# Performance work log

Measured on AMD Instinct MI355X. Metric: run time of the kernel, lower is better.

The kernel has to match this reference:

```python
import jax, jax.numpy as jnp
import numpy as np

B = 256
IN_F = 4096
OUT_F = 4096
NNZ_T = 500_000
NNZ_N = 100_000


def setup_inputs() -> dict:
    key = jax.random.key(0)
    k1, k2, k3, k4, k5, k6 = jax.random.split(key, 6)
    x = jax.random.normal(k1, (B, IN_F), dtype=jnp.float32)
    st_idx = jax.random.randint(k2, (2, NNZ_T), 0, OUT_F, dtype=jnp.int64)  # row in [0,OUT_F), col in [0,IN_F); both 4096
    st_vals = jax.random.normal(k3, (NNZ_T,), dtype=jnp.float32) * (1.0 / np.sqrt(IN_F))
    sn_idx = jax.random.randint(k4, (2, NNZ_N), 0, OUT_F, dtype=jnp.int64)
    sn_vals = jax.random.normal(k5, (NNZ_N,), dtype=jnp.float32) * (1.0 / np.sqrt(IN_F))
    b = jax.random.normal(k6, (OUT_F,), dtype=jnp.float32) * 0.01
    return {"x": x, "st_idx": st_idx, "st_vals": st_vals,
            "sn_idx": sn_idx, "sn_vals": sn_vals, "b": b}


def _spmm_t(x, idx, vals, out_features):
    """Compute x @ A^T where A is COO sparse with idx=(rows, cols), vals.
    A has shape (out_features, in_features). Returns (batch, out_features).
    Duplicate indices are summed, matching torch coalesce semantics."""
    rows, cols = idx[0], idx[1]
    contrib = x[:, cols] * vals[None, :]            # (B, nnz)
    y = jax.ops.segment_sum(contrib.T, rows, num_segments=out_features)  # (out, B)
    return y.T                                       # (B, out)


def reference(x, st_idx, st_vals, sn_idx, sn_vals, b):
    out_features = b.shape[0]
    # y = x @ (S_T + S_N)^T + b == x @ S_T^T + x @ S_N^T + b
    y = _spmm_t(x, st_idx, st_vals, out_features)
    y = y + _spmm_t(x, sn_idx, sn_vals, out_features)
    return y + b[None, :]
```

## Files before the change

### kernel.cpp

```cpp
#include <hip/hip_runtime.h>

#define IN_FT   4096
#define OUT_FT  4096
#define B_SZ    256
#define NNZ_T   500000
#define NNZ_N   100000
#define NNZ_TOT 600000
#define QTR_N   150000
#define QTR4    (QTR_N / 2)
#define ROWS_PB 64
#define QROW_CAP 256
#define ACC_LD  257

#define OFF_ENT  0u
#define OFF_XT   4800000u
#define OFF_FLAG 8994304u

__global__ __launch_bounds__(256) void k_init(const float* __restrict__ bias,
                                              float* __restrict__ out,
                                              const int* __restrict__ st_idx,
                                              const int* __restrict__ sn_idx,
                                              int* __restrict__ flag) {
    int i = blockIdx.x * 256 + threadIdx.x;
    float4* out4 = (float4*)out;
    const float4* bias4 = (const float4*)bias;
    out4[i] = bias4[i & 1023];
    if (blockIdx.x == 0) {
        __shared__ int nz_t, nz_n;
        if (threadIdx.x == 0) { nz_t = 0; nz_n = 0; }
        __syncthreads();
        if (st_idx[2 * threadIdx.x + 1] != 0) atomicAdd(&nz_t, 1);
        if (sn_idx[2 * threadIdx.x + 1] != 0) atomicAdd(&nz_n, 1);
        __syncthreads();
        if (threadIdx.x == 0) { flag[0] = (nz_t == 0); flag[1] = (nz_n == 0); }
    }
}

__global__ __launch_bounds__(256) void k_transpose(const float* __restrict__ in,
                                                   float* __restrict__ out,
                                                   int rows, int cols) {
    __shared__ float tile[32][33];
    int x0 = blockIdx.x * 32;
    int y0 = blockIdx.y * 32;
    int tx = threadIdx.x, ty = threadIdx.y;
    #pragma unroll
    for (int j = 0; j < 32; j += 8)
        tile[ty + j][tx] = in[(size_t)(y0 + ty + j) * cols + (x0 + tx)];
    __syncthreads();
    #pragma unroll
    for (int j = 0; j < 32; j += 8)
        out[(size_t)(x0 + ty + j) * rows + (y0 + tx)] = tile[tx][ty + j];
}

__device__ __forceinline__ void get_entry(int i,
                                          const int* __restrict__ st_idx,
                                          const float* __restrict__ st_vals,
                                          const int* __restrict__ sn_idx,
                                          const float* __restrict__ sn_vals,
                                          int stride_t, int stride_n,
                                          int& row, int& col, float& val) {
    if (i < NNZ_T) {
        row = st_idx[(size_t)i * stride_t];
        col = st_idx[(size_t)(NNZ_T + i) * stride_t];
        val = st_vals[i];
    } else {
        int j = i - NNZ_T;
        row = sn_idx[(size_t)j * stride_n];
        col = sn_idx[(size_t)(NNZ_N + j) * stride_n];
        val = sn_vals[j];
    }
}

__global__ __launch_bounds__(256) void k_pack(const int* __restrict__ st_idx,
                                              const float* __restrict__ st_vals,
                                              const int* __restrict__ sn_idx,
                                              const float* __restrict__ sn_vals,
                                              const int* __restrict__ flag,
                                              uint2* __restrict__ ent) {
    int i = blockIdx.x * 256 + threadIdx.x;
    if (i >= NNZ_TOT) return;
    int s_t = flag[0] ? 2 : 1, s_n = flag[1] ? 2 : 1;
    int row, col; float val;
    get_entry(i, st_idx, st_vals, sn_idx, sn_vals, s_t, s_n, row, col, val);
    ent[i] = make_uint2(((unsigned)row << 12) | (unsigned)col, __float_as_uint(val));
}

__global__ __launch_bounds__(1024) void k_gf(const float* __restrict__ xT,
                                             const uint2* __restrict__ ent,
                                             float* __restrict__ out) {
    extern __shared__ char smem[];
    uint2* queues = (uint2*)smem;
    float* acc    = (float*)smem;
    __shared__ int cnt_s[ROWS_PB];
    const int t = threadIdx.x;
    const int lane = t & 63;
    const int wave = t >> 6;
    const int qi = blockIdx.x & 3;
    const unsigned R0 = (unsigned)(blockIdx.x >> 2) * ROWS_PB;

    if (t < ROWS_PB) cnt_s[t] = 0;
    __syncthreads();

    const uint4* ep = (const uint4*)(ent + (size_t)qi * QTR_N);
    for (int i = t; i < QTR4; i += 1024) {
        uint4 e = ep[i];
        unsigned r0 = (e.x >> 12) - R0;
        if (r0 < (unsigned)ROWS_PB) {
            int p = atomicAdd(&cnt_s[r0], 1);
            if (p < QROW_CAP) queues[r0 * QROW_CAP + p] = make_uint2(e.x, e.y);
        }
        unsigned r1 = (e.z >> 12) - R0;
        if (r1 < (unsigned)ROWS_PB) {
            int p = atomicAdd(&cnt_s[r1], 1);
            if (p < QROW_CAP) queues[r1 * QROW_CAP + p] = make_uint2(e.z, e.w);
        }
    }
    __syncthreads();

    float4 av0 = {0.f,0.f,0.f,0.f}, av1 = av0, av2 = av0, av3 = av0;
    {
        const int q = wave * 4;
        const int n0 = min(cnt_s[q + 0], QROW_CAP);
        const int n1 = min(cnt_s[q + 1], QROW_CAP);
        const int n2 = min(cnt_s[q + 2], QROW_CAP);
        const int n3 = min(cnt_s[q + 3], QROW_CAP);
        const uint2* q0 = queues + (q + 0) * QROW_CAP;
        const uint2* q1 = queues + (q + 1) * QROW_CAP;
        const uint2* q2 = queues + (q + 2) * QROW_CAP;
        const uint2* q3 = queues + (q + 3) * QROW_CAP;
        const int nmax = max(max(n0, n1), max(n2, n3));
        #pragma unroll 2
        for (int j = 0; j < nmax; ++j) {
            uint2 e0 = (j < n0) ? q0[j] : make_uint2(0u, 0u);
            uint2 e1 = (j < n1) ? q1[j] : make_uint2(0u, 0u);
            uint2 e2 = (j < n2) ? q2[j] : make_uint2(0u, 0u);
            uint2 e3 = (j < n3) ? q3[j] : make_uint2(0u, 0u);
            const float4* p0 = (const float4*)(xT + (size_t)(e0.x & 4095u) * B_SZ);
            const float4* p1 = (const float4*)(xT + (size_t)(e1.x & 4095u) * B_SZ);
            const float4* p2 = (const float4*)(xT + (size_t)(e2.x & 4095u) * B_SZ);
            const float4* p3 = (const float4*)(xT + (size_t)(e3.x & 4095u) * B_SZ);
            float4 x0 = p0[lane];
            float4 x1 = p1[lane];
            float4 x2 = p2[lane];
            float4 x3 = p3[lane];
            float v0 = __uint_as_float(e0.y);
            float v1 = __uint_as_float(e1.y);
            float v2 = __uint_as_float(e2.y);
            float v3 = __uint_as_float(e3.y);
            av0.x = fmaf(v0, x0.x, av0.x); av0.y = fmaf(v0, x0.y, av0.y);
            av0.z = fmaf(v0, x0.z, av0.z); av0.w = fmaf(v0, x0.w, av0.w);
            av1.x = fmaf(v1, x1.x, av1.x); av1.y = fmaf(v1, x1.y, av1.y);
            av1.z = fmaf(v1, x1.z, av1.z); av1.w = fmaf(v1, x1.w, av1.w);
            av2.x = fmaf(v2, x2.x, av2.x); av2.y = fmaf(v2, x2.y, av2.y);
            av2.z = fmaf(v2, x2.z, av2.z); av2.w = fmaf(v2, x2.w, av2.w);
            av3.x = fmaf(v3, x3.x, av3.x); av3.y = fmaf(v3, x3.y, av3.y);
            av3.z = fmaf(v3, x3.z, av3.z); av3.w = fmaf(v3, x3.w, av3.w);
        }
    }
    __syncthreads();

    {
        float* a0 = acc + (wave * 4 + 0) * ACC_LD + 4 * lane;
        float* a1 = acc + (wave * 4 + 1) * ACC_LD + 4 * lane;
        float* a2 = acc + (wave * 4 + 2) * ACC_LD + 4 * lane;
        float* a3 = acc + (wave * 4 + 3) * ACC_LD + 4 * lane;
        a0[0] = av0.x; a0[1] = av0.y; a0[2] = av0.z; a0[3] = av0.w;
        a1[0] = av1.x; a1[1] = av1.y; a1[2] = av1.z; a1[3] = av1.w;
        a2[0] = av2.x; a2[1] = av2.y; a2[2] = av2.z; a2[3] = av2.w;
        a3[0] = av3.x; a3[1] = av3.y; a3[2] = av3.z; a3[3] = av3.w;
    }
    __syncthreads();

    #pragma unroll
    for (int k = 0; k < 16; ++k) {
        int cell = t + k * 1024;
        int rr = cell & 63, b = cell >> 6;
        unsafeAtomicAdd(&out[(size_t)b * OUT_FT + R0 + rr], acc[rr * ACC_LD + b]);
    }
}

extern "C" void kernel_launch(void* const* d_in, const int* in_sizes, int n_in,
                              void* d_out, int out_size, void* d_ws, size_t ws_size,
                              hipStream_t stream) {
    const float* x       = (const float*)d_in[0];
    const int*   st_idx  = (const int*)d_in[1];
    const float* st_vals = (const float*)d_in[2];
    const int*   sn_idx  = (const int*)d_in[3];
    const float* sn_vals = (const float*)d_in[4];
    const float* bias    = (const float*)d_in[5];
    float* out = (float*)d_out;

    char* ws = (char*)d_ws;
    uint2* ent  = (uint2*)(ws + OFF_ENT);
    float* xT   = (float*)(ws + OFF_XT);
    int*   flag = (int*)  (ws + OFF_FLAG);

    (void)hipFuncSetAttribute((const void*)k_gf,
                              hipFuncAttributeMaxDynamicSharedMemorySize, 131072);

    k_init<<<(B_SZ * OUT_FT / 4) / 256, 256, 0, stream>>>(bias, out, st_idx, sn_idx, flag);
    k_transpose<<<dim3(IN_FT / 32, B_SZ / 32), dim3(32, 8), 0, stream>>>(x, xT, B_SZ, IN_FT);
    k_pack<<<(NNZ_TOT + 255) / 256, 256, 0, stream>>>(st_idx, st_vals, sn_idx, sn_vals,
                                                      flag, ent);
    k_gf<<<256, 1024, 131072, stream>>>(xT, ent, out);
}
```

Before: 141.3 us.

## Batch gather loads in k_gf, zero-pad queues, halve LDS, stagger output atomics

The gather loop now runs in steps of four, fetching sixteen queue entries and then issuing sixteen independent xT float4 loads before any FMA, so more memory requests are in flight per wave. Queues are zero-filled up front, which lets padded slots read as column 0 with value 0 and removes the per-element bounds predicates. The per-row queue cap drops from 256 to 128, cutting dynamic LDS to about 64 KB; a row with more than 128 entries in one quarter would now be silently dropped. The final atomic-add loop is rotated by quarter index so the four blocks that share output rows hit different addresses at the same time, reducing atomic contention.

```diff
diff --git a/kernel.cpp b/kernel.cpp
--- a/kernel.cpp
+++ b/kernel.cpp
@@ -9,7 +9,7 @@
 #define QTR_N   150000
 #define QTR4    (QTR_N / 2)
 #define ROWS_PB 64
-#define QROW_CAP 256
+#define QROW_CAP 128
 #define ACC_LD  257
 
 #define OFF_ENT  0u
@@ -98,6 +98,8 @@
     const int qi = blockIdx.x & 3;
     const unsigned R0 = (unsigned)(blockIdx.x >> 2) * ROWS_PB;
 
+    #pragma unroll
+    for (int k = 0; k < 8; ++k) queues[t + k * 1024] = make_uint2(0u, 0u);
     if (t < ROWS_PB) cnt_s[t] = 0;
     __syncthreads();
 
@@ -128,33 +130,35 @@
         const uint2* q1 = queues + (q + 1) * QROW_CAP;
         const uint2* q2 = queues + (q + 2) * QROW_CAP;
         const uint2* q3 = queues + (q + 3) * QROW_CAP;
-        const int nmax = max(max(n0, n1), max(n2, n3));
-        #pragma unroll 2
-        for (int j = 0; j < nmax; ++j) {
-            uint2 e0 = (j < n0) ? q0[j] : make_uint2(0u, 0u);
-            uint2 e1 = (j < n1) ? q1[j] : make_uint2(0u, 0u);
-            uint2 e2 = (j < n2) ? q2[j] : make_uint2(0u, 0u);
-            uint2 e3 = (j < n3) ? q3[j] : make_uint2(0u, 0u);
-            const float4* p0 = (const float4*)(xT + (size_t)(e0.x & 4095u) * B_SZ);
-            const float4* p1 = (const float4*)(xT + (size_t)(e1.x & 4095u) * B_SZ);
-            const float4* p2 = (const float4*)(xT + (size_t)(e2.x & 4095u) * B_SZ);
-            const float4* p3 = (const float4*)(xT + (size_t)(e3.x & 4095u) * B_SZ);
-            float4 x0 = p0[lane];
-            float4 x1 = p1[lane];
-            float4 x2 = p2[lane];
-            float4 x3 = p3[lane];
-            float v0 = __uint_as_float(e0.y);
-            float v1 = __uint_as_float(e1.y);
-            float v2 = __uint_as_float(e2.y);
-            float v3 = __uint_as_float(e3.y);
-            av0.x = fmaf(v0, x0.x, av0.x); av0.y = fmaf(v0, x0.y, av0.y);
-            av0.z = fmaf(v0, x0.z, av0.z); av0.w = fmaf(v0, x0.w, av0.w);
-            av1.x = fmaf(v1, x1.x, av1.x); av1.y = fmaf(v1, x1.y, av1.y);
-            av1.z = fmaf(v1, x1.z, av1.z); av1.w = fmaf(v1, x1.w, av1.w);
-            av2.x = fmaf(v2, x2.x, av2.x); av2.y = fmaf(v2, x2.y, av2.y);
-            av2.z = fmaf(v2, x2.z, av2.z); av2.w = fmaf(v2, x2.w, av2.w);
-            av3.x = fmaf(v3, x3.x, av3.x); av3.y = fmaf(v3, x3.y, av3.y);
-            av3.z = fmaf(v3, x3.z, av3.z); av3.w = fmaf(v3, x3.w, av3.w);
+        const int nmax4 = (max(max(n0, n1), max(n2, n3)) + 3) & ~3;
+        for (int j = 0; j < nmax4; j += 4) {
+            uint2 e[16];
+            #pragma unroll
+            for (int u = 0; u < 4; ++u) {
+                e[0 * 4 + u] = q0[j + u];
+                e[1 * 4 + u] = q1[j + u];
+                e[2 * 4 + u] = q2[j + u];
+                e[3 * 4 + u] = q3[j + u];
+            }
+            float4 xv[16];
+            #pragma unroll
+            for (int k = 0; k < 16; ++k)
+                xv[k] = ((const float4*)(xT + (size_t)(e[k].x & 4095u) * B_SZ))[lane];
+            #pragma unroll
+            for (int u = 0; u < 4; ++u) {
+                float v0 = __uint_as_float(e[0 * 4 + u].y);
+                float v1 = __uint_as_float(e[1 * 4 + u].y);
+                float v2 = __uint_as_float(e[2 * 4 + u].y);
+                float v3 = __uint_as_float(e[3 * 4 + u].y);
+                av0.x = fmaf(v0, xv[0*4+u].x, av0.x); av0.y = fmaf(v0, xv[0*4+u].y, av0.y);
+                av0.z = fmaf(v0, xv[0*4+u].z, av0.z); av0.w = fmaf(v0, xv[0*4+u].w, av0.w);
+                av1.x = fmaf(v1, xv[1*4+u].x, av1.x); av1.y = fmaf(v1, xv[1*4+u].y, av1.y);
+                av1.z = fmaf(v1, xv[1*4+u].z, av1.z); av1.w = fmaf(v1, xv[1*4+u].w, av1.w);
+                av2.x = fmaf(v2, xv[2*4+u].x, av2.x); av2.y = fmaf(v2, xv[2*4+u].y, av2.y);
+                av2.z = fmaf(v2, xv[2*4+u].z, av2.z); av2.w = fmaf(v2, xv[2*4+u].w, av2.w);
+                av3.x = fmaf(v3, xv[3*4+u].x, av3.x); av3.y = fmaf(v3, xv[3*4+u].y, av3.y);
+                av3.z = fmaf(v3, xv[3*4+u].z, av3.z); av3.w = fmaf(v3, xv[3*4+u].w, av3.w);
+            }
         }
     }
     __syncthreads();
@@ -172,7 +176,8 @@
     __syncthreads();
 
     #pragma unroll
-    for (int k = 0; k < 16; ++k) {
+    for (int kk = 0; kk < 16; ++kk) {
+        int k = (kk + qi * 4) & 15;
         int cell = t + k * 1024;
         int rr = cell & 63, b = cell >> 6;
         unsafeAtomicAdd(&out[(size_t)b * OUT_FT + R0 + rr], acc[rr * ACC_LD + b]);
@@ -196,11 +201,11 @@
     int*   flag = (int*)  (ws + OFF_FLAG);
 
     (void)hipFuncSetAttribute((const void*)k_gf,
-                              hipFuncAttributeMaxDynamicSharedMemorySize, 131072);
+                              hipFuncAttributeMaxDynamicSharedMemorySize, 65792);
 
     k_init<<<(B_SZ * OUT_FT / 4) / 256, 256, 0, stream>>>(bias, out, st_idx, sn_idx, flag);
     k_transpose<<<dim3(IN_FT / 32, B_SZ / 32), dim3(32, 8), 0, stream>>>(x, xT, B_SZ, IN_FT);
     k_pack<<<(NNZ_TOT + 255) / 256, 256, 0, stream>>>(st_idx, st_vals, sn_idx, sn_vals,
                                                       flag, ent);
-    k_gf<<<256, 1024, 131072, stream>>>(xT, ent, out);
-}
+    k_gf<<<256, 1024, 65792, stream>>>(xT, ent, out);
+}
```

New measurement: 144.3 us. 2.1% more time.
